# Kernel optimization log

Hardware: AMD Instinct MI355X
Metric: run time of the kernel (lower is better)

Reference implementation:

```python
import jax, jax.numpy as jnp
import numpy as np

# Dimensions: [B, head, ci_per_head, H, W]; rfft over last two dims.
B, H, CI, CO, S0, S1, M = 32, 8, 64, 64, 32, 64, 256
F1 = S1 // 2 + 1  # 33 rfft bins on last dim
SCALE = 1.0 / (512 * 512)  # 1/(in_channels*out_channels)


def setup_inputs() -> dict:
    key = jax.random.key(0)
    k1, k2, k3 = jax.random.split(key, 3)
    x = jax.random.normal(k1, (B, H, CI, S0, S1), dtype=jnp.float32)
    # torch.rand(..., dtype=cfloat) -> uniform[0,1) real and imag parts
    w_real = SCALE * jax.random.uniform(k2, (H, CI, CO, M), dtype=jnp.float32)
    w_imag = SCALE * jax.random.uniform(k3, (H, CI, CO, M), dtype=jnp.float32)
    # 'random' mode selection: 256 distinct flat indices into the S0*F1 rfft grid
    rng = np.random.default_rng(0)
    mask_idx = jnp.asarray(np.sort(rng.choice(S0 * F1, M, replace=False)).astype(np.int32))
    return {"x": x, "w_real": w_real, "w_imag": w_imag, "mask_idx": mask_idx}


def reference(x, w_real, w_imag, mask_idx):
    W = (w_real + 1j * w_imag).astype(jnp.complex64)  # (H, CI, CO, M)
    x_ft = jnp.fft.rfftn(x, axes=(3, 4), norm='ortho')  # (B,H,CI,S0,F1) complex64
    xf = x_ft.reshape(B, H, CI, S0 * F1)
    xm = jnp.take(xf, mask_idx, axis=-1)              # gather active modes (B,H,CI,M)
    om = jnp.einsum('bhil,hiol->bhol', xm, W)          # per-mode complex linear map
    out = jnp.zeros((B, H, CO, S0 * F1), dtype=jnp.complex64).at[..., mask_idx].set(om)
    out = out.reshape(B, H, CO, S0, F1)
    # canonical_fft_freq over freq dims except the rfft (last) dim: here only dim 3.
    # indexes/indexes2 form a full permutation pairing j <-> (-j) mod S0, so the
    # in-place averaging equals new[j] = (old[j] + conj(old[-j mod S0])) / 2.
    perm = (-jnp.arange(S0)) % S0
    out = 0.5 * (out + jnp.conj(out[:, :, :, perm, :]))
    y = jnp.fft.irfftn(out, s=(S0, S1), axes=(3, 4), norm='ortho')  # (B,H,CO,S0,S1) real
    return y
```

## Files before the change

### kernel.cpp

```cpp
#include <hip/hip_runtime.h>

#define F1 33

constexpr float TWD[64] = {
   1.00000000f,  0.99518473f,  0.98078528f,  0.95694034f,
   0.92387953f,  0.88192126f,  0.83146961f,  0.77301045f,
   0.70710678f,  0.63439328f,  0.55557023f,  0.47139674f,
   0.38268343f,  0.29028468f,  0.19509032f,  0.09801714f,
   0.00000000f, -0.09801714f, -0.19509032f, -0.29028468f,
  -0.38268343f, -0.47139674f, -0.55557023f, -0.63439328f,
  -0.70710678f, -0.77301045f, -0.83146961f, -0.88192126f,
  -0.92387953f, -0.95694034f, -0.98078528f, -0.99518473f,
  -1.00000000f, -0.99518473f, -0.98078528f, -0.95694034f,
  -0.92387953f, -0.88192126f, -0.83146961f, -0.77301045f,
  -0.70710678f, -0.63439328f, -0.55557023f, -0.47139674f,
  -0.38268343f, -0.29028468f, -0.19509032f, -0.09801714f,
   0.00000000f,  0.09801714f,  0.19509032f,  0.29028468f,
   0.38268343f,  0.47139674f,  0.55557023f,  0.63439328f,
   0.70710678f,  0.77301045f,  0.83146961f,  0.88192126f,
   0.92387953f,  0.95694034f,  0.98078528f,  0.99518473f,
};

__global__ __launch_bounds__(256) void k_sort(const int* __restrict__ mask,
                                              int* __restrict__ sorted,
                                              int* __restrict__ invperm) {
  __shared__ int ks[256];
  __shared__ int sv[256];
  __shared__ int skey[256];
  int t = threadIdx.x;
  int mi = mask[t];
  int j = mi / F1;
  int k = mi - j * F1;
  ks[t] = k;
  __syncthreads();
  int mykey = (k << 8) | t;
  int rank = 0;
  for (int l2 = 0; l2 < 256; ++l2)
    rank += (((ks[l2] << 8) | l2) < mykey);
  sv[rank]   = (k << 16) | (j << 8) | t;
  skey[rank] = k;
  invperm[t] = rank;
  __syncthreads();
  int isend = (t == 255) || (skey[t] != skey[t + 1]);
  sorted[t] = sv[t] | (isend << 24);
}

__global__ __launch_bounds__(256, 4) void k_fwd(const float* __restrict__ x,
                                                const int* __restrict__ sorted,
                                                float2* __restrict__ xm) {
  __shared__ float2 rbuf[128][35];
  __shared__ float2 cs32[32];
  int t = threadIdx.x;
  if (t < 32) cs32[t] = make_float2(TWD[(2 * t) & 63], TWD[(2 * t + 48) & 63]);

  int rl  = t >> 1;
  int par = t & 1;
  size_t row = (size_t)blockIdx.x * 128 + rl;
  const float4* xp = (const float4*)(x + row * 64);

  float f[32];
#pragma unroll
  for (int q = 0; q < 16; ++q) {
    float4 v = xp[q];
    f[2 * q + 0] = par ? v.y : v.x;
    f[2 * q + 1] = par ? v.w : v.z;
  }

  float s1v[16], d1v[16];
#pragma unroll
  for (int m = 0; m < 16; ++m) {
    s1v[m] = f[m] + f[m + 16];
    d1v[m] = f[m] - f[m + 16];
  }
  float s2v[8], d2v[8];
#pragma unroll
  for (int m = 0; m < 8; ++m) {
    s2v[m] = s1v[m] + s1v[m + 8];
    d2v[m] = s1v[m] - s1v[m + 8];
  }
  float mR[17], mI[17];
#pragma unroll
  for (int j = 0; j < 17; ++j) { mR[j] = 0.f; mI[j] = 0.f; }
#pragma unroll
  for (int m = 0; m < 8; ++m) {
#pragma unroll
    for (int tq = 0; tq < 5; ++tq) {
      const int j = 4 * tq;
      const int a = (2 * j * m) & 63;
      const float c  = TWD[a];
      const float sn = TWD[(a + 48) & 63];
      if (c  != 0.0f) mR[j] = fmaf(s2v[m],  c,  mR[j]);
      if (sn != 0.0f) mI[j] = fmaf(s2v[m], -sn, mI[j]);
    }
  }
#pragma unroll
  for (int m = 0; m < 8; ++m) {
#pragma unroll
    for (int tq = 0; tq < 4; ++tq) {
      const int j = 4 * tq + 2;
      const int a = (2 * j * m) & 63;
      const float c  = TWD[a];
      const float sn = TWD[(a + 48) & 63];
      if (c  != 0.0f) mR[j] = fmaf(d2v[m],  c,  mR[j]);
      if (sn != 0.0f) mI[j] = fmaf(d2v[m], -sn, mI[j]);
    }
  }
#pragma unroll
  for (int m = 0; m < 16; ++m) {
#pragma unroll
    for (int r = 0; r < 8; ++r) {
      const int j = 2 * r + 1;
      const int a = (2 * j * m) & 63;
      const float c  = TWD[a];
      const float sn = TWD[(a + 48) & 63];
      if (c  != 0.0f) mR[j] = fmaf(d1v[m],  c,  mR[j]);
      if (sn != 0.0f) mI[j] = fmaf(d1v[m], -sn, mI[j]);
    }
  }

  float oR[17], oI[17];
#pragma unroll
  for (int j = 0; j < 17; ++j) {
    oR[j] = __shfl_xor(mR[j], 1, 64);
    oI[j] = __shfl_xor(mI[j], 1, 64);
  }

  if (par == 0) {
#pragma unroll
    for (int k = 0; k <= 16; ++k) {
      const float wr = TWD[k];
      const float s  = TWD[(k + 48) & 63];
      float XR = mR[k];
      float XI = mI[k];
      if (s  != 0.0f) { XR = fmaf( s, oI[k], XR); XI = fmaf(-s, oR[k], XI); }
      if (wr != 0.0f) { XR = fmaf(wr, oR[k], XR); XI = fmaf(wr, oI[k], XI); }
      rbuf[rl][k] = make_float2(XR, XI);
    }
  } else {
#pragma unroll
    for (int k = 17; k <= 31; ++k) {
      const float wr = TWD[k];
      const float s  = TWD[(k + 48) & 63];
      const int p = 32 - k;
      float XR = oR[p];
      float XI = -oI[p];
      if (s  != 0.0f) { XR = fmaf(-s, mI[p], XR); XI = fmaf(-s, mR[p], XI); }
      if (wr != 0.0f) { XR = fmaf(wr, mR[p], XR); XI = fmaf(-wr, mI[p], XI); }
      rbuf[rl][k] = make_float2(XR, XI);
    }
    rbuf[rl][32] = make_float2(oR[0] - mR[0], 0.0f);
  }
  __syncthreads();

  int e = sorted[t];
  int k = (e >> 16) & 63, j = (e >> 8) & 255, l = e & 255;
  float2 acc[4];
#pragma unroll
  for (int u = 0; u < 4; ++u) acc[u] = make_float2(0.f, 0.f);

#pragma unroll 4
  for (int s0 = 0; s0 < 32; ++s0) {
    float2 cs = cs32[(j * s0) & 31];
#pragma unroll
    for (int u = 0; u < 4; ++u) {
      float2 rv = rbuf[u * 32 + s0][k];
      acc[u].x = fmaf(rv.x, cs.x, fmaf(rv.y,  cs.y, acc[u].x));
      acc[u].y = fmaf(rv.y, cs.x, fmaf(-rv.x, cs.y, acc[u].y));
    }
  }
  size_t ub = (size_t)blockIdx.x * 4;
#pragma unroll
  for (int u = 0; u < 4; ++u)
    xm[(ub + u) * 256 + l] = acc[u];
}

__global__ __launch_bounds__(512, 2) void k_mix(const float2* __restrict__ xm,
                                                const float* __restrict__ wr,
                                                const float* __restrict__ wi,
                                                float2* __restrict__ om) {
  __shared__ float4 Asm4[8][4][33];
  __shared__ float4 Wsm4[8][65][4];
  int t = threadIdx.x;
  int h  = blockIdx.x >> 5;
  int lb = (blockIdx.x & 31) * 8;

  int w    = t >> 6;
  int lane = t & 63;
  int b_lo = lane >> 2;
  int o_lo = lane & 3;

  float4 acc[2][2][4];
#pragma unroll
  for (int brp = 0; brp < 2; ++brp)
#pragma unroll
    for (int orp = 0; orp < 2; ++orp)
#pragma unroll
      for (int p = 0; p < 4; ++p)
        acc[brp][orp][p] = make_float4(0.f, 0.f, 0.f, 0.f);

  for (int ic = 0; ic < 8; ++ic) {
    __syncthreads();
#pragma unroll
    for (int q = 0; q < 2; ++q) {
      int c = t + 512 * q;
      int p = c & 3, ii = (c >> 2) & 7, b = c >> 5;
      const float4* src = (const float4*)(xm +
          (size_t)(((b * 8 + h) * 64) + ic * 8 + ii) * 256 + lb + 2 * p);
      Asm4[ii][p][b] = *src;
    }
#pragma unroll
    for (int q = 0; q < 2; ++q) {
      int c = t + 512 * q;
      int p2 = c & 1, oo = (c >> 1) & 63, ii = c >> 7;
      size_t gidx = (size_t)((h * 64 + ic * 8 + ii) * 64 + oo) * 256 + lb + p2 * 4;
      float4 vr = *(const float4*)(wr + gidx);
      float4 vi = *(const float4*)(wi + gidx);
      Wsm4[ii][oo][2 * p2 + 0] = make_float4(vr.x, vi.x, vr.y, vi.y);
      Wsm4[ii][oo][2 * p2 + 1] = make_float4(vr.z, vi.z, vr.w, vi.w);
    }
    __syncthreads();
#pragma unroll
    for (int i = 0; i < 8; ++i) {
      float4 av[2][4], wv[2][4];
#pragma unroll
      for (int brp = 0; brp < 2; ++brp)
#pragma unroll
        for (int p = 0; p < 4; ++p)
          av[brp][p] = Asm4[i][p][brp * 16 + b_lo];
#pragma unroll
      for (int orp = 0; orp < 2; ++orp)
#pragma unroll
        for (int p = 0; p < 4; ++p)
          wv[orp][p] = Wsm4[i][w * 8 + orp * 4 + o_lo][p];
#pragma unroll
      for (int brp = 0; brp < 2; ++brp)
#pragma unroll
        for (int orp = 0; orp < 2; ++orp)
#pragma unroll
          for (int p = 0; p < 4; ++p) {
            float4 A = av[brp][p], W = wv[orp][p];
            float4& C = acc[brp][orp][p];
            C.x = fmaf(A.x, W.x, fmaf(-A.y, W.y, C.x));
            C.y = fmaf(A.x, W.y, fmaf( A.y, W.x, C.y));
            C.z = fmaf(A.z, W.z, fmaf(-A.w, W.w, C.z));
            C.w = fmaf(A.z, W.w, fmaf( A.w, W.z, C.w));
          }
    }
  }
#pragma unroll
  for (int brp = 0; brp < 2; ++brp)
#pragma unroll
    for (int orp = 0; orp < 2; ++orp)
#pragma unroll
      for (int p = 0; p < 4; ++p) {
        int b = brp * 16 + b_lo;
        int o = w * 8 + orp * 4 + o_lo;
        *(float4*)(om + (size_t)(((b * 8 + h) * 64) + o) * 256 + lb + 2 * p)
            = acc[brp][orp][p];
      }
}

__global__ __launch_bounds__(512, 4) void k_inv(const float2* __restrict__ om,
                                                const int* __restrict__ sorted,
                                                const int* __restrict__ invperm,
                                                float* __restrict__ y) {
  __shared__ float4 om8s[8 * 128];
  __shared__ float  c2s[33][64];
  __shared__ float2 cs32[32];
  __shared__ int4   smodes4[64];
  int t = threadIdx.x;
  size_t ub = (size_t)blockIdx.x * 8;

  {
    int l  = t & 255;
    int u0 = t >> 8;
    int pos = invperm[l];
    float2* dst = (float2*)om8s;
    const float2* omg = om + ub * 256;
#pragma unroll
    for (int q = 0; q < 4; ++q) {
      int u = u0 + 2 * q;
      dst[u * 256 + pos] = omg[u * 256 + l];
    }
  }
#pragma unroll
  for (int q = 0; q < 5; ++q) {
    int idx = t + 512 * q;
    if (idx < 2112) {
      int k = idx >> 6, s1 = idx & 63;
      float w = (k == 0 || k == 32) ? (1.0f / 2048.0f) : (2.0f / 2048.0f);
      c2s[k][s1] = w * TWD[(k * s1) & 63];
    }
  }
  if (t < 32) cs32[t] = make_float2(TWD[(2 * t) & 63], TWD[(2 * t + 48) & 63]);
  if (t < 64) smodes4[t] = ((const int4*)sorted)[t];
  __syncthreads();

  int u    = t >> 6;
  int a    = (t >> 1) & 31;
  int half = t & 1;

  float4 a0 = make_float4(0.f,0.f,0.f,0.f), a1 = a0, a2 = a0, a3 = a0;
  float4 a4 = a0, a5 = a0, a6 = a0, a7 = a0;
  float g = 0.f;

#define SPREAD(KK)                                                            \
  do {                                                                        \
    const float4* crow = (const float4*)&c2s[(KK)][half * 32];                \
    float4 c;                                                                 \
    c = crow[0]; a0.x=fmaf(g,c.x,a0.x); a0.y=fmaf(g,c.y,a0.y); a0.z=fmaf(g,c.z,a0.z); a0.w=fmaf(g,c.w,a0.w); \
    c = crow[1]; a1.x=fmaf(g,c.x,a1.x); a1.y=fmaf(g,c.y,a1.y); a1.z=fmaf(g,c.z,a1.z); a1.w=fmaf(g,c.w,a1.w); \
    c = crow[2]; a2.x=fmaf(g,c.x,a2.x); a2.y=fmaf(g,c.y,a2.y); a2.z=fmaf(g,c.z,a2.z); a2.w=fmaf(g,c.w,a2.w); \
    c = crow[3]; a3.x=fmaf(g,c.x,a3.x); a3.y=fmaf(g,c.y,a3.y); a3.z=fmaf(g,c.z,a3.z); a3.w=fmaf(g,c.w,a3.w); \
    c = crow[4]; a4.x=fmaf(g,c.x,a4.x); a4.y=fmaf(g,c.y,a4.y); a4.z=fmaf(g,c.z,a4.z); a4.w=fmaf(g,c.w,a4.w); \
    c = crow[5]; a5.x=fmaf(g,c.x,a5.x); a5.y=fmaf(g,c.y,a5.y); a5.z=fmaf(g,c.z,a5.z); a5.w=fmaf(g,c.w,a5.w); \
    c = crow[6]; a6.x=fmaf(g,c.x,a6.x); a6.y=fmaf(g,c.y,a6.y); a6.z=fmaf(g,c.z,a6.z); a6.w=fmaf(g,c.w,a6.w); \
    c = crow[7]; a7.x=fmaf(g,c.x,a7.x); a7.y=fmaf(g,c.y,a7.y); a7.z=fmaf(g,c.z,a7.z); a7.w=fmaf(g,c.w,a7.w); \
    g = 0.f;                                                                  \
  } while (0)

#define PROC(EV, OVR, OVI)                                                    \
  do {                                                                        \
    int e_ = (EV);                                                            \
    int j_ = (e_ >> 8) & 255;                                                 \
    float2 cs_ = cs32[(j_ * a) & 31];                                         \
    g = fmaf((OVR), cs_.x, g);                                                \
    g = fmaf(-(OVI), cs_.y, g);                                               \
    if (e_ & (1 << 24)) SPREAD((e_ >> 16) & 63);                              \
  } while (0)

#pragma unroll 2
  for (int q = 0; q < 64; ++q) {
    int4   ee = smodes4[q];
    float4 oA = om8s[u * 128 + 2 * q + 0];
    float4 oB = om8s[u * 128 + 2 * q + 1];
    PROC(ee.x, oA.x, oA.y);
    PROC(ee.y, oA.z, oA.w);
    PROC(ee.z, oB.x, oB.y);
    PROC(ee.w, oB.z, oB.w);
  }
#undef PROC
#undef SPREAD

  float4* yp = (float4*)(y + (ub + u) * 2048 + a * 64 + half * 32);
  yp[0] = a0; yp[1] = a1; yp[2] = a2; yp[3] = a3;
  yp[4] = a4; yp[5] = a5; yp[6] = a6; yp[7] = a7;
}

extern "C" void kernel_launch(void* const* d_in, const int* in_sizes, int n_in,
                              void* d_out, int out_size, void* d_ws, size_t ws_size,
                              hipStream_t stream) {
  const float* x    = (const float*)d_in[0];
  const float* wre  = (const float*)d_in[1];
  const float* wim  = (const float*)d_in[2];
  const int*   mask = (const int*)d_in[3];

  float*  y  = (float*)d_out;
  float2* xm = (float2*)d_out;
  float2* omp = (float2*)d_ws;
  char* base = (char*)d_ws;
  int*  sorted  = (int*)(base + 33554432);
  int*  invperm = (int*)(base + 33555456);

  k_sort<<<1, 256, 0, stream>>>(mask, sorted, invperm);
  k_fwd <<<4096, 256, 0, stream>>>(x, sorted, xm);
  k_mix <<<256, 512, 0, stream>>>(xm, wre, wim, omp);
  k_inv <<<2048, 512, 0, stream>>>(omp, sorted, invperm, y);
}
```

Before: 238.6 us.

## Split inverse FFT into column-DFT and row-DFT kernels via workspace intermediate

Replaces the single fused inverse kernel with two kernels. The first applies the inverse column DFT over sparse modes and writes a k-major intermediate of 33 bins per row to workspace. The second applies the real inverse DFT along the last dim using compile-time twiddle constants. This aims to cut per-block register and shared-memory pressure and the redundant per-unit work of the fused kernel, at the cost of an extra round trip of roughly 69 MB through global memory. The old path is kept as a fallback when the workspace is too small.

```diff
diff --git a/kernel.cpp b/kernel.cpp
--- a/kernel.cpp
+++ b/kernel.cpp
@@ -21,6 +21,8 @@
    0.92387953f,  0.95694034f,  0.98078528f,  0.99518473f,
 };
 
+#define NROWS 524288
+
 __global__ __launch_bounds__(256) void k_sort(const int* __restrict__ mask,
                                               int* __restrict__ sorted,
                                               int* __restrict__ invperm) {
@@ -258,6 +260,123 @@
         *(float4*)(om + (size_t)(((b * 8 + h) * 64) + o) * 256 + lb + 2 * p)
             = acc[brp][orp][p];
       }
+}
+
+__global__ __launch_bounds__(256, 4) void k_inv_a(const float2* __restrict__ om,
+                                                  const int* __restrict__ sorted,
+                                                  const int* __restrict__ invperm,
+                                                  float* __restrict__ T) {
+  __shared__ float4 om16s[16 * 128];
+  __shared__ float2 cs32[32];
+  __shared__ int4   smodes4[64];
+  int t = threadIdx.x;
+  size_t ub = (size_t)blockIdx.x * 16;
+
+  {
+    int pos = invperm[t];
+    float2* dst = (float2*)om16s;
+    const float2* omg = om + ub * 256;
+#pragma unroll
+    for (int u = 0; u < 16; ++u)
+      dst[u * 256 + pos] = omg[u * 256 + t];
+  }
+  if (t < 32) cs32[t] = make_float2(TWD[(2 * t) & 63], TWD[(2 * t + 48) & 63]);
+  if (t < 64) smodes4[t] = ((const int4*)sorted)[t];
+  __syncthreads();
+
+  int up = t >> 5;
+  int a  = t & 31;
+  int u0 = up * 2, u1 = u0 + 1;
+  float g0 = 0.f, g1 = 0.f;
+  long long seen = 0;
+
+#define PROC2(EV, R0, I0, R1, I1)                                             \
+  do {                                                                        \
+    int e_ = (EV);                                                            \
+    int j_ = (e_ >> 8) & 255;                                                 \
+    float2 cs_ = cs32[(j_ * a) & 31];                                         \
+    g0 = fmaf((R0), cs_.x, g0); g0 = fmaf(-(I0), cs_.y, g0);                  \
+    g1 = fmaf((R1), cs_.x, g1); g1 = fmaf(-(I1), cs_.y, g1);                  \
+    if (e_ & (1 << 24)) {                                                     \
+      int k_ = (e_ >> 16) & 63;                                               \
+      seen |= 1ll << k_;                                                      \
+      T[(size_t)k_ * NROWS + (ub + u0) * 32 + a] = g0;                        \
+      T[(size_t)k_ * NROWS + (ub + u1) * 32 + a] = g1;                        \
+      g0 = 0.f; g1 = 0.f;                                                     \
+    }                                                                         \
+  } while (0)
+
+#pragma unroll 2
+  for (int q = 0; q < 64; ++q) {
+    int4   ee  = smodes4[q];
+    float4 oA0 = om16s[u0 * 128 + 2 * q + 0];
+    float4 oB0 = om16s[u0 * 128 + 2 * q + 1];
+    float4 oA1 = om16s[u1 * 128 + 2 * q + 0];
+    float4 oB1 = om16s[u1 * 128 + 2 * q + 1];
+    PROC2(ee.x, oA0.x, oA0.y, oA1.x, oA1.y);
+    PROC2(ee.y, oA0.z, oA0.w, oA1.z, oA1.w);
+    PROC2(ee.z, oB0.x, oB0.y, oB1.x, oB1.y);
+    PROC2(ee.w, oB0.z, oB0.w, oB1.z, oB1.w);
+  }
+#undef PROC2
+
+#pragma unroll
+  for (int k = 0; k < 33; ++k)
+    if (!((seen >> k) & 1)) {
+      T[(size_t)k * NROWS + (ub + u0) * 32 + a] = 0.f;
+      T[(size_t)k * NROWS + (ub + u1) * 32 + a] = 0.f;
+    }
+}
+
+template <int SG>
+__device__ __forceinline__ void inv_b_body(const float (*T8)[34], int r,
+                                           float* __restrict__ y, size_t Rb) {
+  float acc[16];
+  {
+    float t0 = T8[r][0];
+#pragma unroll
+    for (int o = 0; o < 16; ++o)
+      acc[o] = t0 * (1.0f / 2048.0f);
+  }
+#pragma unroll
+  for (int k = 1; k < 33; ++k) {
+    float tk = T8[r][k];
+#pragma unroll
+    for (int o = 0; o < 16; ++o) {
+      const float C = ((k == 32) ? (1.0f / 2048.0f) : (2.0f / 2048.0f))
+                    * TWD[(k * (SG * 16 + o)) & 63];
+      if (C != 0.0f) acc[o] = fmaf(tk, C, acc[o]);
+    }
+  }
+  float* yp = y + (Rb + r) * 64 + SG * 16;
+#pragma unroll
+  for (int q = 0; q < 4; ++q)
+    *(float4*)(yp + 4 * q) = make_float4(acc[4 * q + 0], acc[4 * q + 1],
+                                         acc[4 * q + 2], acc[4 * q + 3]);
+}
+
+__global__ __launch_bounds__(256, 4) void k_inv_b(const float* __restrict__ T,
+                                                  float* __restrict__ y) {
+  __shared__ float T8[64][34];
+  int t = threadIdx.x;
+  size_t Rb = (size_t)blockIdx.x * 64;
+
+#pragma unroll
+  for (int q = 0; q < 9; ++q) {
+    int c = t + 256 * q;
+    if (c < 2112) {
+      int kq = c >> 6, r = c & 63;
+      T8[r][kq] = T[(size_t)kq * NROWS + Rb + r];
+    }
+  }
+  __syncthreads();
+
+  int wv = t >> 6;
+  int r  = t & 63;
+  if      (wv == 0) inv_b_body<0>(T8, r, y, Rb);
+  else if (wv == 1) inv_b_body<1>(T8, r, y, Rb);
+  else if (wv == 2) inv_b_body<2>(T8, r, y, Rb);
+  else              inv_b_body<3>(T8, r, y, Rb);
 }
 
 __global__ __launch_bounds__(512, 4) void k_inv(const float2* __restrict__ om,
@@ -361,9 +480,16 @@
   char* base = (char*)d_ws;
   int*  sorted  = (int*)(base + 33554432);
   int*  invperm = (int*)(base + 33555456);
+  float* T      = (float*)(base + 33556480);
+  const size_t ws_needed = 33556480ull + (size_t)33 * NROWS * 4;
 
   k_sort<<<1, 256, 0, stream>>>(mask, sorted, invperm);
   k_fwd <<<4096, 256, 0, stream>>>(x, sorted, xm);
   k_mix <<<256, 512, 0, stream>>>(xm, wre, wim, omp);
-  k_inv <<<2048, 512, 0, stream>>>(omp, sorted, invperm, y);
-}
+  if (ws_size >= ws_needed) {
+    k_inv_a<<<1024, 256, 0, stream>>>(omp, sorted, invperm, T);
+    k_inv_b<<<8192, 256, 0, stream>>>(T, y);
+  } else {
+    k_inv<<<2048, 512, 0, stream>>>(omp, sorted, invperm, y);
+  }
+}
```

New measurement: 227.9 us. 4.5% less time.
